# Optimization experiments

Measured on AMD Instinct MI355X. Metric: run time of the kernel, lower is better.

## Reference

```python
import jax, jax.numpy as jnp
import numpy as np


def _conv1x1(x, W, b):
    # 1x1 conv == per-pixel channel matmul: x [B,C,H,W], W [O,C], b [O]
    return jnp.einsum('bchw,oc->bohw', x, W) + b[None, :, None, None]


def setup_inputs() -> dict:
    key = jax.random.key(0)
    ks = jax.random.split(key, 9)
    B, C, H, W = 16, 512, 32, 32
    s = 1.0 / np.sqrt(C)
    inp = {
        'x': jax.random.normal(ks[0], (B, C, H, W), dtype=jnp.float32),
        'Wq': jax.random.normal(ks[1], (C, C), dtype=jnp.float32) * s,
        'bq': jax.random.normal(ks[2], (C,), dtype=jnp.float32) * 0.01,
        'Wk': jax.random.normal(ks[3], (C, C), dtype=jnp.float32) * s,
        'bk': jax.random.normal(ks[4], (C,), dtype=jnp.float32) * 0.01,
        'Wv': jax.random.normal(ks[5], (C, C), dtype=jnp.float32) * s,
        'bv': jax.random.normal(ks[6], (C,), dtype=jnp.float32) * 0.01,
        'Wo': jax.random.normal(ks[7], (C, C), dtype=jnp.float32) * s,
        'bo': jax.random.normal(ks[8], (C,), dtype=jnp.float32) * 0.01,
    }
    return inp


def reference(x, Wq, bq, Wk, bk, Wv, bv, Wo, bo):
    B, C, H, W = x.shape
    q = _conv1x1(x, Wq, bq)
    k = _conv1x1(x, Wk, bk)
    v = _conv1x1(x, Wv, bv)
    hw = H * W
    qf = q.reshape(B, C, hw)  # [B,C,HW]
    kf = k.reshape(B, C, hw)
    vf = v.reshape(B, C, hw)
    # scores[b,i,j] = sum_c q[b,c,i] * k[b,c,j], scaled by c^-0.5
    scores = jnp.einsum('bci,bcj->bij', qf, kf) * (C ** -0.5)
    attn = jax.nn.softmax(scores, axis=2)  # softmax over keys j
    # out[b,c,i] = sum_j v[b,c,j] * attn[b,i,j]
    out = jnp.einsum('bcj,bij->bci', vf, attn).reshape(B, C, H, W)
    out = _conv1x1(out, Wo, bo)
    return x + out
```

## Files before the change

kernel.cpp:

```cpp
#include <hip/hip_runtime.h>
#include <hip/hip_bf16.h>
#include <math.h>


typedef __bf16 bf16x8 __attribute__((ext_vector_type(8)));
typedef float  f32x4  __attribute__((ext_vector_type(4)));

__device__ __forceinline__ unsigned short f2bf(float f) {
    unsigned u = __float_as_uint(f);
    u += 0x7fff + ((u >> 16) & 1);
    return (unsigned short)(u >> 16);
}

__device__ __forceinline__ void gload_lds16(const void* g, void* l) {
    __builtin_amdgcn_global_load_lds(
        (const __attribute__((address_space(1))) void*)g,
        (__attribute__((address_space(3))) void*)l, 16, 0, 0);
}

template<bool OUT_F32, int BIAS_MODE, bool RESID>
__global__ __launch_bounds__(256) void gemm_bt_mfma(
    const unsigned short* __restrict__ A, const unsigned short* __restrict__ B,
    void* __restrict__ Cout, const float* __restrict__ bias,
    const float* __restrict__ resid,
    int M, int N, int K, long sA, long sB, long sC, long sR)
{
    __shared__ unsigned short Als[128 * 32];
    __shared__ unsigned short Bls[128 * 32];

    const int bz = blockIdx.z;
    A += bz * sA;
    B += bz * sB;
    const int m0 = blockIdx.y * 128;
    const int n0 = blockIdx.x * 128;

    const int tid  = threadIdx.x;
    const int lane = tid & 63;
    const int wave = tid >> 6;
    const int wm   = wave >> 1;
    const int wn   = wave & 1;

    const int ar = lane >> 2;
    const int ak = (lane & 3) * 8;

    const unsigned short* agp0 = A + (long)(m0 + wave * 16 + ar) * K + ak;
    const unsigned short* agp1 = agp0 + 64L * K;
    const unsigned short* bgp0 = B + (long)(n0 + wave * 16 + ar) * K + ak;
    const unsigned short* bgp1 = bgp0 + 64L * K;
    unsigned short* al0 = Als + wave * 512;
    unsigned short* al1 = Als + (wave + 4) * 512;
    unsigned short* bl0 = Bls + wave * 512;
    unsigned short* bl1 = Bls + (wave + 4) * 512;

    const int fr = lane & 15;
    const int fq = lane >> 4;

    f32x4 acc[4][4] = {};

    for (int k0 = 0; k0 < K; k0 += 32) {
        gload_lds16(agp0, al0);
        gload_lds16(agp1, al1);
        gload_lds16(bgp0, bl0);
        gload_lds16(bgp1, bl1);
        agp0 += 32; agp1 += 32; bgp0 += 32; bgp1 += 32;
        __syncthreads();

        bf16x8 af[4], bfr[4];
        #pragma unroll
        for (int mt = 0; mt < 4; ++mt)
            af[mt] = *(const bf16x8*)&Als[(wm * 64 + mt * 16 + fr) * 32 + fq * 8];
        #pragma unroll
        for (int nt = 0; nt < 4; ++nt)
            bfr[nt] = *(const bf16x8*)&Bls[(wn * 64 + nt * 16 + fr) * 32 + fq * 8];

        #pragma unroll
        for (int mt = 0; mt < 4; ++mt)
            #pragma unroll
            for (int nt = 0; nt < 4; ++nt)
                acc[mt][nt] = __builtin_amdgcn_mfma_f32_16x16x32_bf16(
                    af[mt], bfr[nt], acc[mt][nt], 0, 0, 0);
        __syncthreads();
    }

    float* Cf = (float*)Cout + bz * sC;
    unsigned short* Ch = (unsigned short*)Cout + bz * sC;
    if (RESID) resid += bz * sR;

    #pragma unroll
    for (int nt = 0; nt < 4; ++nt) {
        const int col = n0 + wn * 64 + nt * 16 + fr;
        const float bn = (BIAS_MODE == 2) ? bias[col] : 0.0f;
        #pragma unroll
        for (int mt = 0; mt < 4; ++mt) {
            const int row = m0 + wm * 64 + mt * 16 + fq * 4;
            #pragma unroll
            for (int r = 0; r < 4; ++r) {
                float val = acc[mt][nt][r] + bn;
                if (BIAS_MODE == 1) val += bias[row + r];
                const long idx = (long)(row + r) * N + col;
                if (RESID) val += resid[idx];
                if (OUT_F32) Cf[idx] = val;
                else         Ch[idx] = f2bf(val);
            }
        }
    }
}

__global__ __launch_bounds__(256) void transpose_cast(
    const float* __restrict__ x, unsigned short* __restrict__ xT)
{
    __shared__ float t[32][33];
    const int b = blockIdx.z;
    const int p0 = blockIdx.x * 32;
    const int c0 = blockIdx.y * 32;
    const float* xb = x + (long)b * 524288;
    unsigned short* xTb = xT + (long)b * 524288;
    const int tx = threadIdx.x & 31;
    const int ty = threadIdx.x >> 5;
    #pragma unroll
    for (int i = 0; i < 4; ++i)
        t[ty + 8 * i][tx] = xb[(long)(c0 + ty + 8 * i) * 1024 + p0 + tx];
    __syncthreads();
    #pragma unroll
    for (int i = 0; i < 4; ++i)
        xTb[(long)(p0 + ty + 8 * i) * 512 + c0 + tx] = f2bf(t[tx][ty + 8 * i]);
}

__global__ __launch_bounds__(256) void cast_weights(
    const float* __restrict__ w0, const float* __restrict__ w1,
    const float* __restrict__ w2, const float* __restrict__ w3,
    unsigned short* __restrict__ dst)
{
    const float* srcs[4] = {w0, w1, w2, w3};
    const float* s = srcs[blockIdx.y];
    unsigned short* d = dst + (long)blockIdx.y * 262144;
    const int i = (blockIdx.x * 256 + threadIdx.x) * 4;
    const float4 f = *(const float4*)(s + i);
    ushort4 h;
    h.x = f2bf(f.x); h.y = f2bf(f.y); h.z = f2bf(f.z); h.w = f2bf(f.w);
    *(ushort4*)(d + i) = h;
}

__global__ __launch_bounds__(256) void softmax_rows(
    const float* __restrict__ S, unsigned short* __restrict__ P, float scale)
{
    const long row = blockIdx.x;
    const float* s = S + row * 1024L;
    unsigned short* p = P + row * 1024L;
    const int tid = threadIdx.x;
    const int lane = tid & 63;
    const int wid = tid >> 6;

    float v[4];
    float mx = -INFINITY;
    #pragma unroll
    for (int e = 0; e < 4; ++e) {
        v[e] = s[tid + e * 256];
        mx = fmaxf(mx, v[e]);
    }
    #pragma unroll
    for (int off = 32; off > 0; off >>= 1)
        mx = fmaxf(mx, __shfl_down(mx, off));

    __shared__ float redmax[4], redsum[4];
    if (lane == 0) redmax[wid] = mx;
    __syncthreads();
    mx = fmaxf(fmaxf(redmax[0], redmax[1]), fmaxf(redmax[2], redmax[3]));

    float sum = 0.0f;
    #pragma unroll
    for (int e = 0; e < 4; ++e) {
        v[e] = __expf((v[e] - mx) * scale);
        sum += v[e];
    }
    #pragma unroll
    for (int off = 32; off > 0; off >>= 1)
        sum += __shfl_down(sum, off);
    if (lane == 0) redsum[wid] = sum;
    __syncthreads();
    sum = redsum[0] + redsum[1] + redsum[2] + redsum[3];

    const float inv = 1.0f / sum;
    #pragma unroll
    for (int e = 0; e < 4; ++e)
        p[tid + e * 256] = f2bf(v[e] * inv);
}

extern "C" void kernel_launch(void* const* d_in, const int* in_sizes, int n_in,
                              void* d_out, int out_size, void* d_ws, size_t ws_size,
                              hipStream_t stream)
{
    const float* x  = (const float*)d_in[0];
    const float* Wq = (const float*)d_in[1];
    const float* bq = (const float*)d_in[2];
    const float* Wk = (const float*)d_in[3];
    const float* bk = (const float*)d_in[4];
    const float* Wv = (const float*)d_in[5];
    const float* bv = (const float*)d_in[6];
    const float* Wo = (const float*)d_in[7];
    const float* bo = (const float*)d_in[8];
    float* out = (float*)d_out;

    const int Bn = 16, C = 512, HW = 1024;
    const long CHW = (long)C * HW;
    const long SHW = (long)HW * HW;

    unsigned short* xT = (unsigned short*)d_ws;
    unsigned short* qT = xT + Bn * CHW;
    unsigned short* kT = qT + Bn * CHW;
    unsigned short* vB = kT + Bn * CHW;
    float*          Sb = (float*)(vB + Bn * CHW);
    unsigned short* Wb = (unsigned short*)(Sb + Bn * SHW);
    unsigned short* OT = xT;
    unsigned short* P  = qT;

    unsigned short* Wqb = Wb;
    unsigned short* Wkb = Wb + 1 * 262144;
    unsigned short* Wvb = Wb + 2 * 262144;
    unsigned short* Wob = Wb + 3 * 262144;

    const dim3 blk(256);

    cast_weights<<<dim3(256, 4), blk, 0, stream>>>(Wq, Wk, Wv, Wo, Wb);
    transpose_cast<<<dim3(32, 16, Bn), blk, 0, stream>>>(x, xT);

    gemm_bt_mfma<false, 2, false><<<dim3(4, 8, Bn), blk, 0, stream>>>(
        xT, Wqb, qT, bq, nullptr, HW, C, C, CHW, 0, CHW, 0);
    gemm_bt_mfma<false, 2, false><<<dim3(4, 8, Bn), blk, 0, stream>>>(
        xT, Wkb, kT, bk, nullptr, HW, C, C, CHW, 0, CHW, 0);
    gemm_bt_mfma<false, 1, false><<<dim3(8, 4, Bn), blk, 0, stream>>>(
        Wvb, xT, vB, bv, nullptr, C, HW, C, 0, CHW, CHW, 0);

    gemm_bt_mfma<true, 0, false><<<dim3(8, 8, Bn), blk, 0, stream>>>(
        qT, kT, Sb, nullptr, nullptr, HW, HW, C, CHW, CHW, SHW, 0);

    softmax_rows<<<dim3(Bn * HW), blk, 0, stream>>>(Sb, P, 0.044194173824159216f);

    gemm_bt_mfma<false, 0, false><<<dim3(4, 8, Bn), blk, 0, stream>>>(
        P, vB, OT, nullptr, nullptr, HW, C, HW, SHW, CHW, CHW, 0);

    gemm_bt_mfma<true, 1, true><<<dim3(8, 4, Bn), blk, 0, stream>>>(
        Wob, OT, out, bo, x, C, HW, C, 0, CHW, CHW, CHW);
}
```

Baseline: 268.5 us.

## Fuse softmax into score GEMM epilogue and merge Q/K projections

Q and K projections now run as one GEMM over concatenated weights, writing an interleaved qk buffer. The score GEMM's epilogue computes exp(scale*s) directly, stores it as bf16 and atomically accumulates row sums. The PV GEMM then divides by those sums in its epilogue, which removes the fp32 score matrix and the separate softmax pass. Because no max is subtracted, the exp can overflow for large logits, and the atomics add some contention.

```diff
diff --git a/kernel.cpp b/kernel.cpp
--- a/kernel.cpp
+++ b/kernel.cpp
@@ -18,12 +18,13 @@
         (__attribute__((address_space(3))) void*)l, 16, 0, 0);
 }
 
-template<bool OUT_F32, int BIAS_MODE, bool RESID>
+template<bool OUT_F32, int BIAS_MODE, bool RESID, int EXPM>
 __global__ __launch_bounds__(256) void gemm_bt_mfma(
     const unsigned short* __restrict__ A, const unsigned short* __restrict__ B,
     void* __restrict__ Cout, const float* __restrict__ bias,
-    const float* __restrict__ resid,
-    int M, int N, int K, long sA, long sB, long sC, long sR)
+    const float* __restrict__ resid, float* __restrict__ lsum,
+    int M, int N, int K, int ldA, int ldB,
+    long sA, long sB, long sC, long sR, float scale)
 {
     __shared__ unsigned short Als[128 * 32];
     __shared__ unsigned short Bls[128 * 32];
@@ -43,10 +44,10 @@
     const int ar = lane >> 2;
     const int ak = (lane & 3) * 8;
 
-    const unsigned short* agp0 = A + (long)(m0 + wave * 16 + ar) * K + ak;
-    const unsigned short* agp1 = agp0 + 64L * K;
-    const unsigned short* bgp0 = B + (long)(n0 + wave * 16 + ar) * K + ak;
-    const unsigned short* bgp1 = bgp0 + 64L * K;
+    const unsigned short* agp0 = A + (long)(m0 + wave * 16 + ar) * ldA + ak;
+    const unsigned short* agp1 = agp0 + 64L * ldA;
+    const unsigned short* bgp0 = B + (long)(n0 + wave * 16 + ar) * ldB + ak;
+    const unsigned short* bgp1 = bgp0 + 64L * ldB;
     unsigned short* al0 = Als + wave * 512;
     unsigned short* al1 = Als + (wave + 4) * 512;
     unsigned short* bl0 = Bls + wave * 512;
@@ -86,21 +87,55 @@
     unsigned short* Ch = (unsigned short*)Cout + bz * sC;
     if (RESID) resid += bz * sR;
 
-    #pragma unroll
-    for (int nt = 0; nt < 4; ++nt) {
-        const int col = n0 + wn * 64 + nt * 16 + fr;
-        const float bn = (BIAS_MODE == 2) ? bias[col] : 0.0f;
+    if (EXPM == 1) {
+        float* lrow = lsum + bz * (long)M;
         #pragma unroll
         for (int mt = 0; mt < 4; ++mt) {
             const int row = m0 + wm * 64 + mt * 16 + fq * 4;
             #pragma unroll
             for (int r = 0; r < 4; ++r) {
-                float val = acc[mt][nt][r] + bn;
-                if (BIAS_MODE == 1) val += bias[row + r];
-                const long idx = (long)(row + r) * N + col;
-                if (RESID) val += resid[idx];
-                if (OUT_F32) Cf[idx] = val;
-                else         Ch[idx] = f2bf(val);
+                float rs = 0.0f;
+                #pragma unroll
+                for (int nt = 0; nt < 4; ++nt) {
+                    const int col = n0 + wn * 64 + nt * 16 + fr;
+                    const float e = __expf(acc[mt][nt][r] * scale);
+                    rs += e;
+                    Ch[(long)(row + r) * N + col] = f2bf(e);
+                }
+                rs += __shfl_xor(rs, 1);
+                rs += __shfl_xor(rs, 2);
+                rs += __shfl_xor(rs, 4);
+                rs += __shfl_xor(rs, 8);
+                if (fr == 0) atomicAdd(&lrow[row + r], rs);
+            }
+        }
+    } else {
+        float linv[4][4];
+        if (EXPM == 2) {
+            const float* lrow = lsum + bz * (long)M;
+            #pragma unroll
+            for (int mt = 0; mt < 4; ++mt)
+                #pragma unroll
+                for (int r = 0; r < 4; ++r)
+                    linv[mt][r] = 1.0f / lrow[m0 + wm * 64 + mt * 16 + fq * 4 + r];
+        }
+        #pragma unroll
+        for (int nt = 0; nt < 4; ++nt) {
+            const int col = n0 + wn * 64 + nt * 16 + fr;
+            const float bn = (BIAS_MODE == 2) ? bias[col] : 0.0f;
+            #pragma unroll
+            for (int mt = 0; mt < 4; ++mt) {
+                const int row = m0 + wm * 64 + mt * 16 + fq * 4;
+                #pragma unroll
+                for (int r = 0; r < 4; ++r) {
+                    float val = acc[mt][nt][r] + bn;
+                    if (BIAS_MODE == 1) val += bias[row + r];
+                    if (EXPM == 2) val *= linv[mt][r];
+                    const long idx = (long)(row + r) * N + col;
+                    if (RESID) val += resid[idx];
+                    if (OUT_F32) Cf[idx] = val;
+                    else         Ch[idx] = f2bf(val);
+                }
             }
         }
     }
@@ -126,64 +161,32 @@
         xTb[(long)(p0 + ty + 8 * i) * 512 + c0 + tx] = f2bf(t[tx][ty + 8 * i]);
 }
 
-__global__ __launch_bounds__(256) void cast_weights(
-    const float* __restrict__ w0, const float* __restrict__ w1,
-    const float* __restrict__ w2, const float* __restrict__ w3,
-    unsigned short* __restrict__ dst)
-{
-    const float* srcs[4] = {w0, w1, w2, w3};
-    const float* s = srcs[blockIdx.y];
-    unsigned short* d = dst + (long)blockIdx.y * 262144;
-    const int i = (blockIdx.x * 256 + threadIdx.x) * 4;
-    const float4 f = *(const float4*)(s + i);
-    ushort4 h;
-    h.x = f2bf(f.x); h.y = f2bf(f.y); h.z = f2bf(f.z); h.w = f2bf(f.w);
-    *(ushort4*)(d + i) = h;
-}
-
-__global__ __launch_bounds__(256) void softmax_rows(
-    const float* __restrict__ S, unsigned short* __restrict__ P, float scale)
-{
-    const long row = blockIdx.x;
-    const float* s = S + row * 1024L;
-    unsigned short* p = P + row * 1024L;
-    const int tid = threadIdx.x;
-    const int lane = tid & 63;
-    const int wid = tid >> 6;
-
-    float v[4];
-    float mx = -INFINITY;
-    #pragma unroll
-    for (int e = 0; e < 4; ++e) {
-        v[e] = s[tid + e * 256];
-        mx = fmaxf(mx, v[e]);
+__global__ __launch_bounds__(256) void prep(
+    const float* __restrict__ Wq, const float* __restrict__ Wk,
+    const float* __restrict__ Wv, const float* __restrict__ Wo,
+    const float* __restrict__ bq, const float* __restrict__ bk,
+    unsigned short* __restrict__ Wb, float* __restrict__ biasqk,
+    float* __restrict__ lsum)
+{
+    const int b = blockIdx.x;
+    const int t = threadIdx.x;
+    if (b < 1024) {
+        const float* srcs[4] = {Wq, Wk, Wv, Wo};
+        const float* s = srcs[b >> 8];
+        unsigned short* d = Wb + (long)(b >> 8) * 262144;
+        const int i = ((b & 255) * 256 + t) * 4;
+        const float4 f = *(const float4*)(s + i);
+        ushort4 h;
+        h.x = f2bf(f.x); h.y = f2bf(f.y); h.z = f2bf(f.z); h.w = f2bf(f.w);
+        *(ushort4*)(d + i) = h;
+    } else {
+        biasqk[t]       = bq[t];
+        biasqk[256 + t] = bq[256 + t];
+        biasqk[512 + t] = bk[t];
+        biasqk[768 + t] = bk[256 + t];
+        #pragma unroll
+        for (int i = 0; i < 64; ++i) lsum[i * 256 + t] = 0.0f;
     }
-    #pragma unroll
-    for (int off = 32; off > 0; off >>= 1)
-        mx = fmaxf(mx, __shfl_down(mx, off));
-
-    __shared__ float redmax[4], redsum[4];
-    if (lane == 0) redmax[wid] = mx;
-    __syncthreads();
-    mx = fmaxf(fmaxf(redmax[0], redmax[1]), fmaxf(redmax[2], redmax[3]));
-
-    float sum = 0.0f;
-    #pragma unroll
-    for (int e = 0; e < 4; ++e) {
-        v[e] = __expf((v[e] - mx) * scale);
-        sum += v[e];
-    }
-    #pragma unroll
-    for (int off = 32; off > 0; off >>= 1)
-        sum += __shfl_down(sum, off);
-    if (lane == 0) redsum[wid] = sum;
-    __syncthreads();
-    sum = redsum[0] + redsum[1] + redsum[2] + redsum[3];
-
-    const float inv = 1.0f / sum;
-    #pragma unroll
-    for (int e = 0; e < 4; ++e)
-        p[tid + e * 256] = f2bf(v[e] * inv);
 }
 
 extern "C" void kernel_launch(void* const* d_in, const int* in_sizes, int n_in,
@@ -205,40 +208,41 @@
     const long CHW = (long)C * HW;
     const long SHW = (long)HW * HW;
 
-    unsigned short* xT = (unsigned short*)d_ws;
-    unsigned short* qT = xT + Bn * CHW;
-    unsigned short* kT = qT + Bn * CHW;
-    unsigned short* vB = kT + Bn * CHW;
-    float*          Sb = (float*)(vB + Bn * CHW);
-    unsigned short* Wb = (unsigned short*)(Sb + Bn * SHW);
+    unsigned short* xT   = (unsigned short*)d_ws;
+    unsigned short* qkT  = xT + Bn * CHW;
+    unsigned short* vB   = qkT + Bn * SHW;
+    unsigned short* expS = vB + Bn * CHW;
+    unsigned short* Wb   = expS + Bn * SHW;
+    float* biasqk = (float*)(Wb + 4 * 262144);
+    float* lsum   = biasqk + 1024;
     unsigned short* OT = xT;
-    unsigned short* P  = qT;
-
-    unsigned short* Wqb = Wb;
-    unsigned short* Wkb = Wb + 1 * 262144;
+
     unsigned short* Wvb = Wb + 2 * 262144;
     unsigned short* Wob = Wb + 3 * 262144;
 
     const dim3 blk(256);
-
-    cast_weights<<<dim3(256, 4), blk, 0, stream>>>(Wq, Wk, Wv, Wo, Wb);
+    const float scale = 0.044194173824159216f;
+
+    prep<<<dim3(1025), blk, 0, stream>>>(Wq, Wk, Wv, Wo, bq, bk, Wb, biasqk, lsum);
     transpose_cast<<<dim3(32, 16, Bn), blk, 0, stream>>>(x, xT);
 
-    gemm_bt_mfma<false, 2, false><<<dim3(4, 8, Bn), blk, 0, stream>>>(
-        xT, Wqb, qT, bq, nullptr, HW, C, C, CHW, 0, CHW, 0);
-    gemm_bt_mfma<false, 2, false><<<dim3(4, 8, Bn), blk, 0, stream>>>(
-        xT, Wkb, kT, bk, nullptr, HW, C, C, CHW, 0, CHW, 0);
-    gemm_bt_mfma<false, 1, false><<<dim3(8, 4, Bn), blk, 0, stream>>>(
-        Wvb, xT, vB, bv, nullptr, C, HW, C, 0, CHW, CHW, 0);
-
-    gemm_bt_mfma<true, 0, false><<<dim3(8, 8, Bn), blk, 0, stream>>>(
-        qT, kT, Sb, nullptr, nullptr, HW, HW, C, CHW, CHW, SHW, 0);
-
-    softmax_rows<<<dim3(Bn * HW), blk, 0, stream>>>(Sb, P, 0.044194173824159216f);
-
-    gemm_bt_mfma<false, 0, false><<<dim3(4, 8, Bn), blk, 0, stream>>>(
-        P, vB, OT, nullptr, nullptr, HW, C, HW, SHW, CHW, CHW, 0);
-
-    gemm_bt_mfma<true, 1, true><<<dim3(8, 4, Bn), blk, 0, stream>>>(
-        Wob, OT, out, bo, x, C, HW, C, 0, CHW, CHW, CHW);
-}
+    gemm_bt_mfma<false, 2, false, 0><<<dim3(8, 8, Bn), blk, 0, stream>>>(
+        xT, Wb, qkT, biasqk, nullptr, nullptr,
+        HW, 2 * C, C, C, C, CHW, 0, SHW, 0, 0.0f);
+
+    gemm_bt_mfma<false, 1, false, 0><<<dim3(8, 4, Bn), blk, 0, stream>>>(
+        Wvb, xT, vB, bv, nullptr, nullptr,
+        C, HW, C, C, C, 0, CHW, CHW, 0, 0.0f);
+
+    gemm_bt_mfma<false, 0, false, 1><<<dim3(8, 8, Bn), blk, 0, stream>>>(
+        qkT, qkT + C, expS, nullptr, nullptr, lsum,
+        HW, HW, C, 2 * C, 2 * C, SHW, SHW, SHW, 0, scale);
+
+    gemm_bt_mfma<false, 0, false, 2><<<dim3(4, 8, Bn), blk, 0, stream>>>(
+        expS, vB, OT, nullptr, nullptr, lsum,
+        HW, C, HW, HW, HW, SHW, CHW, CHW, 0, 0.0f);
+
+    gemm_bt_mfma<true, 1, true, 0><<<dim3(8, 4, Bn), blk, 0, stream>>>(
+        Wob, OT, out, bo, x, nullptr,
+        C, HW, C, C, C, 0, CHW, CHW, CHW, 0.0f);
+}
```

Result: faster. 248.9 us (-7.3%).
